# Performance work log

Measured on AMD Instinct MI355X. Metric: run time of the kernel, lower is better.

## Reference

```python
import jax, jax.numpy as jnp
import numpy as np

N_HEAD = 16
N_EMBED = 1024

def setup_inputs() -> dict:
    key = jax.random.key(0)
    ks = jax.random.split(key, 5)
    C = N_EMBED
    x = jax.random.normal(ks[0], (2, 2048, C), dtype=jnp.float32)
    # c_attn: Linear(C, 3C); c_proj: Linear(C, C). PyTorch Linear: y = x @ W.T + b
    w_attn = jax.random.normal(ks[1], (3 * C, C), dtype=jnp.float32) * (1.0 / np.sqrt(C))
    b_attn = jnp.zeros((3 * C,), dtype=jnp.float32)
    w_proj = jax.random.normal(ks[2], (C, C), dtype=jnp.float32) * (1.0 / np.sqrt(C))
    b_proj = jnp.zeros((C,), dtype=jnp.float32)
    return {"x": x, "w_attn": w_attn, "b_attn": b_attn, "w_proj": w_proj, "b_proj": b_proj}

def reference(x, w_attn, b_attn, w_proj, b_proj):
    B, T, C = x.shape
    H = N_HEAD
    D = C // H
    qkv = jnp.einsum('btc,fc->btf', x, w_attn) + b_attn  # [B,T,3C]
    q, k, v = jnp.split(qkv, 3, axis=-1)
    # [B,H,T,D]
    q = q.reshape(B, T, H, D).transpose(0, 2, 1, 3)
    k = k.reshape(B, T, H, D).transpose(0, 2, 1, 3)
    v = v.reshape(B, T, H, D).transpose(0, 2, 1, 3)
    att = jnp.einsum('bhqd,bhkd->bhqk', q, k) * (1.0 / np.sqrt(D))  # [B,H,T,T]
    causal = jnp.tril(jnp.ones((T, T), dtype=bool))
    att = jnp.where(causal[None, None], att, jnp.finfo(att.dtype).min)
    att = jax.nn.softmax(att, axis=-1)
    y = jnp.einsum('bhqk,bhkd->bhqd', att, v)  # [B,H,T,D]
    y = y.transpose(0, 2, 1, 3).reshape(B, T, C)
    return jnp.einsum('btc,fc->btf', y, w_proj) + b_proj
```

## Files before the change

### kernel.cpp

```cpp
#include <hip/hip_runtime.h>
#include <hip/hip_bf16.h>

typedef unsigned short u16;
typedef __attribute__((ext_vector_type(8))) short v8s;
typedef __attribute__((ext_vector_type(4))) short v4s;
typedef __attribute__((ext_vector_type(4))) float v4f;

#define SCL2 0.180336879f

__device__ __forceinline__ u16 f2bu(float f) {
  union { float f; unsigned u; } v; v.f = f;
  unsigned r = (v.u + 0x7fffu + ((v.u >> 16) & 1u)) >> 16;
  return (u16)r;
}
__device__ __forceinline__ v8s pack8(const v4f& a, const v4f& b) {
  union { v8s s; __hip_bfloat162 h[4]; } u;
  u.h[0] = __float22bfloat162_rn(make_float2(a[0], a[1]));
  u.h[1] = __float22bfloat162_rn(make_float2(a[2], a[3]));
  u.h[2] = __float22bfloat162_rn(make_float2(b[0], b[1]));
  u.h[3] = __float22bfloat162_rn(make_float2(b[2], b[3]));
  return u.s;
}

__device__ __forceinline__ void g2l16(const u16* g, u16* l) {
  __builtin_amdgcn_global_load_lds((const __attribute__((address_space(1))) void*)g,
                                   (__attribute__((address_space(3))) void*)l,
                                   16, 0, 0);
}

__global__ __launch_bounds__(256) void cvt_bf16(const float* __restrict__ s0, u16* __restrict__ d0, int n0,
                                                const float* __restrict__ s1, u16* __restrict__ d1, int n1,
                                                const float* __restrict__ s2, u16* __restrict__ d2, int n2) {
  int total8 = (n0 + n1 + n2) >> 3;
  for (int i = blockIdx.x * blockDim.x + threadIdx.x; i < total8; i += gridDim.x * blockDim.x) {
    int e = i << 3;
    const float* s; u16* d;
    if (e < n0)            { s = s0 + e;            d = d0 + e; }
    else if (e < n0 + n1)  { s = s1 + (e - n0);     d = d1 + (e - n0); }
    else                   { s = s2 + (e - n0 - n1); d = d2 + (e - n0 - n1); }
    v4f a = *(const v4f*)s, b = *(const v4f*)(s + 4);
    *(v8s*)d = pack8(a, b);
  }
}

__global__ __launch_bounds__(256) void gemm_qkv(const u16* __restrict__ A,
                                                const u16* __restrict__ W,
                                                const float* __restrict__ bias,
                                                u16* __restrict__ o0,
                                                u16* __restrict__ o1,
                                                u16* __restrict__ o2) {
  constexpr int K = 1024;
  __shared__ __align__(16) u16 As[128 * 64];
  __shared__ __align__(16) u16 Bs[128 * 64];
  const int tid = threadIdx.x;
  const int w = tid >> 6, lane = tid & 63, l15 = lane & 15, quad = lane >> 4;
  const int wm = w & 1, wn = w >> 1;
  const int R0 = blockIdx.x * 128, C0 = blockIdx.y * 128;

  v4f acc[4][4] = {};
  const u16* Ag = A + (size_t)R0 * K;
  const u16* Wg = W + (size_t)C0 * K;

  int srow[4], scol[4], sdst[4];
#pragma unroll
  for (int i = 0; i < 4; ++i) {
    int p = (w * 4 + i) * 64 + lane;
    srow[i] = p >> 3;
    scol[i] = (p & 7) * 8;
    sdst[i] = (w * 4 + i) * 512;
  }

  for (int k0 = 0; k0 < K; k0 += 64) {
    if (k0) __syncthreads();
#pragma unroll
    for (int i = 0; i < 4; ++i) g2l16(Ag + srow[i] * K + k0 + scol[i], &As[sdst[i]]);
#pragma unroll
    for (int i = 0; i < 4; ++i) g2l16(Wg + srow[i] * K + k0 + scol[i], &Bs[sdst[i]]);
    __syncthreads();
#pragma unroll
    for (int kk = 0; kk < 2; ++kk) {
      v8s a[4], b[4];
#pragma unroll
      for (int m = 0; m < 4; ++m)
        a[m] = *(const v8s*)&As[(wm * 64 + m * 16 + l15) * 64 + (kk * 4 + quad) * 8];
#pragma unroll
      for (int n = 0; n < 4; ++n)
        b[n] = *(const v8s*)&Bs[(wn * 64 + n * 16 + l15) * 64 + (kk * 4 + quad) * 8];
#pragma unroll
      for (int m = 0; m < 4; ++m)
#pragma unroll
        for (int n = 0; n < 4; ++n)
          acc[m][n] = __builtin_amdgcn_mfma_f32_16x16x32_bf16(a[m], b[n], acc[m][n], 0, 0, 0);
    }
  }

#pragma unroll
  for (int n = 0; n < 4; ++n) {
    int f = C0 + wn * 64 + n * 16 + l15;
    float bv = bias[f];
#pragma unroll
    for (int m = 0; m < 4; ++m) {
      int r0 = R0 + wm * 64 + m * 16 + quad * 4;
      int which = f >> 10, c = f & 1023;
      int h = c >> 6, d = c & 63;
      int b = r0 >> 11, t = r0 & 2047;
      if (which == 2) {
        v4s pk;
#pragma unroll
        for (int reg = 0; reg < 4; ++reg) pk[reg] = (short)f2bu(acc[m][n][reg] + bv);
        *(v4s*)&o2[(((b << 4) + h) * 64 + d) * 2048 + t] = pk;
      } else {
        u16* dst = (which == 0) ? o0 : o1;
        float sc = (which == 0) ? SCL2 : 1.0f;
#pragma unroll
        for (int reg = 0; reg < 4; ++reg)
          dst[(((b << 4) + h) * 2048 + (t + reg)) * 64 + d] = f2bu((acc[m][n][reg] + bv) * sc);
      }
    }
  }
}

__global__ __launch_bounds__(256) void gemm_proj(const u16* __restrict__ A,
                                                 const u16* __restrict__ W,
                                                 const float* __restrict__ bias,
                                                 float* __restrict__ out) {
  constexpr int K = 1024;
  __shared__ __align__(16) u16 As[128 * 64];
  __shared__ __align__(16) u16 Bs[64 * 64];
  const int tid = threadIdx.x;
  const int w = tid >> 6, lane = tid & 63, l15 = lane & 15, quad = lane >> 4;
  const int wm = w & 1, wn = w >> 1;
  const int R0 = blockIdx.x * 128, C0 = blockIdx.y * 64;

  v4f acc[4][2] = {};
  const u16* Ag = A + (size_t)R0 * K;
  const u16* Wg = W + (size_t)C0 * K;

  int arow[4], acol[4], adst[4];
#pragma unroll
  for (int i = 0; i < 4; ++i) {
    int p = (w * 4 + i) * 64 + lane;
    arow[i] = p >> 3; acol[i] = (p & 7) * 8; adst[i] = (w * 4 + i) * 512;
  }
  int brow[2], bcol[2], bdst[2];
#pragma unroll
  for (int i = 0; i < 2; ++i) {
    int p = (w * 2 + i) * 64 + lane;
    brow[i] = p >> 3; bcol[i] = (p & 7) * 8; bdst[i] = (w * 2 + i) * 512;
  }

  for (int k0 = 0; k0 < K; k0 += 64) {
    if (k0) __syncthreads();
#pragma unroll
    for (int i = 0; i < 4; ++i) g2l16(Ag + arow[i] * K + k0 + acol[i], &As[adst[i]]);
#pragma unroll
    for (int i = 0; i < 2; ++i) g2l16(Wg + brow[i] * K + k0 + bcol[i], &Bs[bdst[i]]);
    __syncthreads();
#pragma unroll
    for (int kk = 0; kk < 2; ++kk) {
      v8s a[4], b[2];
#pragma unroll
      for (int m = 0; m < 4; ++m)
        a[m] = *(const v8s*)&As[(wm * 64 + m * 16 + l15) * 64 + (kk * 4 + quad) * 8];
#pragma unroll
      for (int n = 0; n < 2; ++n)
        b[n] = *(const v8s*)&Bs[(wn * 32 + n * 16 + l15) * 64 + (kk * 4 + quad) * 8];
#pragma unroll
      for (int m = 0; m < 4; ++m)
#pragma unroll
        for (int n = 0; n < 2; ++n)
          acc[m][n] = __builtin_amdgcn_mfma_f32_16x16x32_bf16(a[m], b[n], acc[m][n], 0, 0, 0);
    }
  }

#pragma unroll
  for (int n = 0; n < 2; ++n) {
    int f = C0 + wn * 32 + n * 16 + l15;
    float bv = bias[f];
#pragma unroll
    for (int m = 0; m < 4; ++m) {
      int r0 = R0 + wm * 64 + m * 16 + quad * 4;
#pragma unroll
      for (int reg = 0; reg < 4; ++reg)
        out[(size_t)(r0 + reg) * 1024 + f] = acc[m][n][reg] + bv;
    }
  }
}

__global__ __launch_bounds__(512, 4) void attn_kernel(const u16* __restrict__ Q,
                                                      const u16* __restrict__ Kt,
                                                      const u16* __restrict__ Vt,
                                                      u16* __restrict__ Y) {
  __shared__ __align__(16) u16 Ksh[2][64 * 64], Vsh[2][64 * 64];
  const int tid = threadIdx.x;
  const int w = tid >> 6, lane = tid & 63, l15 = lane & 15, quad = lane >> 4;
  const int pi = blockIdx.x, h = blockIdx.y, b = blockIdx.z;
  const int myqt = (w < 4) ? pi : 31 - pi;
  const int strip = w & 3;
  const int q0 = myqt * 64 + strip * 16;
  const int KT = 32 - pi;
  const int bh = b * 16 + h;
  const u16* qg = Q + bh * 131072;
  const u16* kg = Kt + bh * 131072;
  const u16* vg = Vt + bh * 131072;

  v8s aq[2];
  {
    const u16* qr = qg + (q0 + l15) * 64;
    aq[0] = *(const v8s*)(qr + quad * 8);
    aq[1] = *(const v8s*)(qr + 32 + quad * 8);
  }

  v4f O[4] = {};
  float ll = 0.f;
  const int rowlim = strip * 16 + l15;

  const int srow = tid >> 3, cc = tid & 7;
  const int sgc = cc * 8, ssc = (cc ^ (srow & 7)) * 8;
  const int vhi = cc >> 1, vlo = cc & 1;
  const int vs0 = srow * 64 + (((vhi * 2)     ^ (srow & 7)) * 8) + vlo * 4;
  const int vs1 = srow * 64 + (((vhi * 2 + 1) ^ (srow & 7)) * 8) + vlo * 4;
  v8s tk = *(const v8s*)(kg + srow * 64 + sgc);
  v8s tv = *(const v8s*)(vg + srow * 2048 + sgc);

  for (int kt = 0; kt < KT; ++kt) {
    const int buf = kt & 1;
    *(v8s*)&Ksh[buf][srow * 64 + ssc] = tk;
    {
      union { v8s v; v4s h[2]; } tvu; tvu.v = tv;
      *(v4s*)&Vsh[buf][vs0] = tvu.h[0];
      *(v4s*)&Vsh[buf][vs1] = tvu.h[1];
    }
    __syncthreads();
    if (kt + 1 < KT) {
      int kn = (kt + 1) * 64;
      tk = *(const v8s*)(kg + (kn + srow) * 64 + sgc);
      tv = *(const v8s*)(vg + srow * 2048 + kn + sgc);
    }
    if (kt <= myqt) {
      const u16* Kb = Ksh[buf];
      const u16* Vb = Vsh[buf];

      v4f s[4];
#pragma unroll
      for (int nt = 0; nt < 4; ++nt) {
        v4f z = {0.f, 0.f, 0.f, 0.f};
#pragma unroll
        for (int kk = 0; kk < 2; ++kk) {
          v8s kf = *(const v8s*)&Kb[(nt * 16 + l15) * 64 + (((kk * 4 + quad) ^ (l15 & 7)) * 8)];
          z = __builtin_amdgcn_mfma_f32_16x16x32_bf16(kf, aq[kk], z, 0, 0, 0);
        }
        s[nt] = z;
      }

      float rs = 0.f;
      if (kt == myqt) {
#pragma unroll
        for (int nt = 0; nt < 4; ++nt)
#pragma unroll
          for (int reg = 0; reg < 4; ++reg) {
            int kl = nt * 16 + quad * 4 + reg;
            float p = (kl <= rowlim) ? exp2f(s[nt][reg]) : 0.f;
            s[nt][reg] = p; rs += p;
          }
      } else {
#pragma unroll
        for (int nt = 0; nt < 4; ++nt)
#pragma unroll
          for (int reg = 0; reg < 4; ++reg) {
            float p = exp2f(s[nt][reg]);
            s[nt][reg] = p; rs += p;
          }
      }
      ll += rs;

      unsigned pk0[4], pk1[4];
#pragma unroll
      for (int nt = 0; nt < 4; ++nt) {
        union { __hip_bfloat162 h; unsigned u; } c0, c1;
        c0.h = __float22bfloat162_rn(make_float2(s[nt][0], s[nt][1]));
        c1.h = __float22bfloat162_rn(make_float2(s[nt][2], s[nt][3]));
        pk0[nt] = c0.u; pk1[nt] = c1.u;
      }
      asm volatile("v_permlane32_swap_b32 %0, %1" : "+v"(pk0[0]), "+v"(pk0[1]));
      asm volatile("v_permlane32_swap_b32 %0, %1" : "+v"(pk1[0]), "+v"(pk1[1]));
      asm volatile("v_permlane32_swap_b32 %0, %1" : "+v"(pk0[2]), "+v"(pk0[3]));
      asm volatile("v_permlane32_swap_b32 %0, %1" : "+v"(pk1[2]), "+v"(pk1[3]));
      v8s ap[2];
      {
        union { v8s v; unsigned u[4]; } a0, a1;
        a0.u[0] = pk0[0]; a0.u[1] = pk1[0]; a0.u[2] = pk0[1]; a0.u[3] = pk1[1];
        a1.u[0] = pk0[2]; a1.u[1] = pk1[2]; a1.u[2] = pk0[3]; a1.u[3] = pk1[3];
        ap[0] = a0.v; ap[1] = a1.v;
      }

#pragma unroll
      for (int nt = 0; nt < 4; ++nt)
#pragma unroll
        for (int kk = 0; kk < 2; ++kk) {
          v8s vf = *(const v8s*)&Vb[(nt * 16 + l15) * 64 + (((kk * 4 + quad) ^ (l15 & 7)) * 8)];
          O[nt] = __builtin_amdgcn_mfma_f32_16x16x32_bf16(ap[kk], vf, O[nt], 0, 0, 0);
        }
    }
  }

  ll += __shfl_xor(ll, 16, 64); ll += __shfl_xor(ll, 32, 64);
  float li = 1.f / ll, lO[4];
#pragma unroll
  for (int reg = 0; reg < 4; ++reg) lO[reg] = __shfl(li, quad * 4 + reg, 64);
  const int tb = q0 + quad * 4;
#pragma unroll
  for (int nt = 0; nt < 4; ++nt)
#pragma unroll
    for (int reg = 0; reg < 4; ++reg)
      Y[(b * 2048 + tb + reg) * 1024 + h * 64 + nt * 16 + l15] = f2bu(O[nt][reg] * lO[reg]);
}

extern "C" void kernel_launch(void* const* d_in, const int* in_sizes, int n_in,
                              void* d_out, int out_size, void* d_ws, size_t ws_size,
                              hipStream_t stream) {
  const float* x      = (const float*)d_in[0];
  const float* w_attn = (const float*)d_in[1];
  const float* b_attn = (const float*)d_in[2];
  const float* w_proj = (const float*)d_in[3];
  const float* b_proj = (const float*)d_in[4];
  float* out = (float*)d_out;
  char* ws = (char*)d_ws;
  u16* xb  = (u16*)(ws);
  u16* wab = (u16*)(ws + (size_t)( 8u << 20));
  u16* wpb = (u16*)(ws + (size_t)(14u << 20));
  u16* q   = (u16*)(ws + (size_t)(16u << 20));
  u16* k   = (u16*)(ws + (size_t)(24u << 20));
  u16* vt  = (u16*)(ws + (size_t)(32u << 20));
  u16* y   = (u16*)(ws + (size_t)(40u << 20));

  cvt_bf16<<<2048, 256, 0, stream>>>(x, xb, 4194304, w_attn, wab, 3145728, w_proj, wpb, 1048576);
  gemm_qkv<<<dim3(32, 24), 256, 0, stream>>>(xb, wab, b_attn, q, k, vt);
  attn_kernel<<<dim3(16, 16, 2), 512, 0, stream>>>(q, k, vt, y);
  gemm_proj<<<dim3(32, 16), 256, 0, stream>>>(y, wpb, b_proj, out);
}
```

Before: 177.1 us.

## Split attention into one block per query tile and read K directly from global

Attention blocks change from 512 threads, each pairing query tile pi with tile 31-pi for load balance, to 256-thread blocks that each handle a single 64-row query tile, with head as the fastest grid dimension. K fragments are now loaded straight from global memory into registers rather than staged through shared memory, so only V stays double-buffered in LDS. This cuts LDS use and per-block synchronisation and raises the block count. In exchange, the causal-triangle work per block is imbalanced and K global reads are less coalesced.

```diff
diff --git a/kernel.cpp b/kernel.cpp
--- a/kernel.cpp
+++ b/kernel.cpp
@@ -187,18 +187,16 @@
   }
 }
 
-__global__ __launch_bounds__(512, 4) void attn_kernel(const u16* __restrict__ Q,
+__global__ __launch_bounds__(256, 4) void attn_kernel(const u16* __restrict__ Q,
                                                       const u16* __restrict__ Kt,
                                                       const u16* __restrict__ Vt,
                                                       u16* __restrict__ Y) {
-  __shared__ __align__(16) u16 Ksh[2][64 * 64], Vsh[2][64 * 64];
+  __shared__ __align__(16) u16 Vsh[2][64 * 64];
   const int tid = threadIdx.x;
   const int w = tid >> 6, lane = tid & 63, l15 = lane & 15, quad = lane >> 4;
-  const int pi = blockIdx.x, h = blockIdx.y, b = blockIdx.z;
-  const int myqt = (w < 4) ? pi : 31 - pi;
-  const int strip = w & 3;
-  const int q0 = myqt * 64 + strip * 16;
-  const int KT = 32 - pi;
+  const int h = blockIdx.x, qt = blockIdx.y, b = blockIdx.z;
+  const int q0 = qt * 64 + w * 16;
+  const int KT = qt + 1;
   const int bh = b * 16 + h;
   const u16* qg = Q + bh * 131072;
   const u16* kg = Kt + bh * 131072;
@@ -213,95 +211,105 @@
 
   v4f O[4] = {};
   float ll = 0.f;
-  const int rowlim = strip * 16 + l15;
-
-  const int srow = tid >> 3, cc = tid & 7;
-  const int sgc = cc * 8, ssc = (cc ^ (srow & 7)) * 8;
-  const int vhi = cc >> 1, vlo = cc & 1;
-  const int vs0 = srow * 64 + (((vhi * 2)     ^ (srow & 7)) * 8) + vlo * 4;
-  const int vs1 = srow * 64 + (((vhi * 2 + 1) ^ (srow & 7)) * 8) + vlo * 4;
-  v8s tk = *(const v8s*)(kg + srow * 64 + sgc);
-  v8s tv = *(const v8s*)(vg + srow * 2048 + sgc);
+  const int rowlim = w * 16 + l15;
+
+  int sg[2], vs0[2], vs1[2];
+#pragma unroll
+  for (int i = 0; i < 2; ++i) {
+    int srow = (tid >> 3) + i * 32, cc = tid & 7;
+    sg[i] = srow * 2048 + cc * 8;
+    int vhi = cc >> 1, vlo = cc & 1;
+    vs0[i] = srow * 64 + (((vhi * 2)     ^ (srow & 7)) * 8) + vlo * 4;
+    vs1[i] = srow * 64 + (((vhi * 2 + 1) ^ (srow & 7)) * 8) + vlo * 4;
+  }
+  v8s tv[2];
+#pragma unroll
+  for (int i = 0; i < 2; ++i) tv[i] = *(const v8s*)(vg + sg[i]);
+
+  const u16* kq = kg + l15 * 64 + quad * 8;
 
   for (int kt = 0; kt < KT; ++kt) {
     const int buf = kt & 1;
-    *(v8s*)&Ksh[buf][srow * 64 + ssc] = tk;
-    {
-      union { v8s v; v4s h[2]; } tvu; tvu.v = tv;
-      *(v4s*)&Vsh[buf][vs0] = tvu.h[0];
-      *(v4s*)&Vsh[buf][vs1] = tvu.h[1];
+#pragma unroll
+    for (int i = 0; i < 2; ++i) {
+      union { v8s v; v4s h[2]; } tvu; tvu.v = tv[i];
+      *(v4s*)&Vsh[buf][vs0[i]] = tvu.h[0];
+      *(v4s*)&Vsh[buf][vs1[i]] = tvu.h[1];
     }
     __syncthreads();
     if (kt + 1 < KT) {
       int kn = (kt + 1) * 64;
-      tk = *(const v8s*)(kg + (kn + srow) * 64 + sgc);
-      tv = *(const v8s*)(vg + srow * 2048 + kn + sgc);
-    }
-    if (kt <= myqt) {
-      const u16* Kb = Ksh[buf];
-      const u16* Vb = Vsh[buf];
-
-      v4f s[4];
-#pragma unroll
-      for (int nt = 0; nt < 4; ++nt) {
-        v4f z = {0.f, 0.f, 0.f, 0.f};
-#pragma unroll
-        for (int kk = 0; kk < 2; ++kk) {
-          v8s kf = *(const v8s*)&Kb[(nt * 16 + l15) * 64 + (((kk * 4 + quad) ^ (l15 & 7)) * 8)];
-          z = __builtin_amdgcn_mfma_f32_16x16x32_bf16(kf, aq[kk], z, 0, 0, 0);
+#pragma unroll
+      for (int i = 0; i < 2; ++i) tv[i] = *(const v8s*)(vg + kn + sg[i]);
+    }
+
+    v8s kf[4][2];
+#pragma unroll
+    for (int nt = 0; nt < 4; ++nt)
+#pragma unroll
+      for (int kk = 0; kk < 2; ++kk)
+        kf[nt][kk] = *(const v8s*)(kq + (kt * 64 + nt * 16) * 64 + kk * 32);
+
+    const u16* Vb = Vsh[buf];
+
+    v4f s[4];
+#pragma unroll
+    for (int nt = 0; nt < 4; ++nt) {
+      v4f z = {0.f, 0.f, 0.f, 0.f};
+#pragma unroll
+      for (int kk = 0; kk < 2; ++kk)
+        z = __builtin_amdgcn_mfma_f32_16x16x32_bf16(kf[nt][kk], aq[kk], z, 0, 0, 0);
+      s[nt] = z;
+    }
+
+    float rs = 0.f;
+    if (kt == qt) {
+#pragma unroll
+      for (int nt = 0; nt < 4; ++nt)
+#pragma unroll
+        for (int reg = 0; reg < 4; ++reg) {
+          int kl = nt * 16 + quad * 4 + reg;
+          float p = (kl <= rowlim) ? exp2f(s[nt][reg]) : 0.f;
+          s[nt][reg] = p; rs += p;
         }
-        s[nt] = z;
+    } else {
+#pragma unroll
+      for (int nt = 0; nt < 4; ++nt)
+#pragma unroll
+        for (int reg = 0; reg < 4; ++reg) {
+          float p = exp2f(s[nt][reg]);
+          s[nt][reg] = p; rs += p;
+        }
+    }
+    ll += rs;
+
+    unsigned pk0[4], pk1[4];
+#pragma unroll
+    for (int nt = 0; nt < 4; ++nt) {
+      union { __hip_bfloat162 h; unsigned u; } c0, c1;
+      c0.h = __float22bfloat162_rn(make_float2(s[nt][0], s[nt][1]));
+      c1.h = __float22bfloat162_rn(make_float2(s[nt][2], s[nt][3]));
+      pk0[nt] = c0.u; pk1[nt] = c1.u;
+    }
+    asm volatile("v_permlane32_swap_b32 %0, %1" : "+v"(pk0[0]), "+v"(pk0[1]));
+    asm volatile("v_permlane32_swap_b32 %0, %1" : "+v"(pk1[0]), "+v"(pk1[1]));
+    asm volatile("v_permlane32_swap_b32 %0, %1" : "+v"(pk0[2]), "+v"(pk0[3]));
+    asm volatile("v_permlane32_swap_b32 %0, %1" : "+v"(pk1[2]), "+v"(pk1[3]));
+    v8s ap[2];
+    {
+      union { v8s v; unsigned u[4]; } a0, a1;
+      a0.u[0] = pk0[0]; a0.u[1] = pk1[0]; a0.u[2] = pk0[1]; a0.u[3] = pk1[1];
+      a1.u[0] = pk0[2]; a1.u[1] = pk1[2]; a1.u[2] = pk0[3]; a1.u[3] = pk1[3];
+      ap[0] = a0.v; ap[1] = a1.v;
+    }
+
+#pragma unroll
+    for (int nt = 0; nt < 4; ++nt)
+#pragma unroll
+      for (int kk = 0; kk < 2; ++kk) {
+        v8s vf = *(const v8s*)&Vb[(nt * 16 + l15) * 64 + (((kk * 4 + quad) ^ (l15 & 7)) * 8)];
+        O[nt] = __builtin_amdgcn_mfma_f32_16x16x32_bf16(ap[kk], vf, O[nt], 0, 0, 0);
       }
-
-      float rs = 0.f;
-      if (kt == myqt) {
-#pragma unroll
-        for (int nt = 0; nt < 4; ++nt)
-#pragma unroll
-          for (int reg = 0; reg < 4; ++reg) {
-            int kl = nt * 16 + quad * 4 + reg;
-            float p = (kl <= rowlim) ? exp2f(s[nt][reg]) : 0.f;
-            s[nt][reg] = p; rs += p;
-          }
-      } else {
-#pragma unroll
-        for (int nt = 0; nt < 4; ++nt)
-#pragma unroll
-          for (int reg = 0; reg < 4; ++reg) {
-            float p = exp2f(s[nt][reg]);
-            s[nt][reg] = p; rs += p;
-          }
-      }
-      ll += rs;
-
-      unsigned pk0[4], pk1[4];
-#pragma unroll
-      for (int nt = 0; nt < 4; ++nt) {
-        union { __hip_bfloat162 h; unsigned u; } c0, c1;
-        c0.h = __float22bfloat162_rn(make_float2(s[nt][0], s[nt][1]));
-        c1.h = __float22bfloat162_rn(make_float2(s[nt][2], s[nt][3]));
-        pk0[nt] = c0.u; pk1[nt] = c1.u;
-      }
-      asm volatile("v_permlane32_swap_b32 %0, %1" : "+v"(pk0[0]), "+v"(pk0[1]));
-      asm volatile("v_permlane32_swap_b32 %0, %1" : "+v"(pk1[0]), "+v"(pk1[1]));
-      asm volatile("v_permlane32_swap_b32 %0, %1" : "+v"(pk0[2]), "+v"(pk0[3]));
-      asm volatile("v_permlane32_swap_b32 %0, %1" : "+v"(pk1[2]), "+v"(pk1[3]));
-      v8s ap[2];
-      {
-        union { v8s v; unsigned u[4]; } a0, a1;
-        a0.u[0] = pk0[0]; a0.u[1] = pk1[0]; a0.u[2] = pk0[1]; a0.u[3] = pk1[1];
-        a1.u[0] = pk0[2]; a1.u[1] = pk1[2]; a1.u[2] = pk0[3]; a1.u[3] = pk1[3];
-        ap[0] = a0.v; ap[1] = a1.v;
-      }
-
-#pragma unroll
-      for (int nt = 0; nt < 4; ++nt)
-#pragma unroll
-        for (int kk = 0; kk < 2; ++kk) {
-          v8s vf = *(const v8s*)&Vb[(nt * 16 + l15) * 64 + (((kk * 4 + quad) ^ (l15 & 7)) * 8)];
-          O[nt] = __builtin_amdgcn_mfma_f32_16x16x32_bf16(ap[kk], vf, O[nt], 0, 0, 0);
-        }
-    }
   }
 
   ll += __shfl_xor(ll, 16, 64); ll += __shfl_xor(ll, 32, 64);
@@ -336,6 +344,6 @@
 
   cvt_bf16<<<2048, 256, 0, stream>>>(x, xb, 4194304, w_attn, wab, 3145728, w_proj, wpb, 1048576);
   gemm_qkv<<<dim3(32, 24), 256, 0, stream>>>(xb, wab, b_attn, q, k, vt);
-  attn_kernel<<<dim3(16, 16, 2), 512, 0, stream>>>(q, k, vt, y);
+  attn_kernel<<<dim3(16, 32, 2), 256, 0, stream>>>(q, k, vt, y);
   gemm_proj<<<dim3(32, 16), 256, 0, stream>>>(y, wpb, b_proj, out);
 }
```

Measured after the change: 239.4 us. +35.2%, slower.
